# Kernel optimization log

Hardware: AMD Instinct MI355X
Metric: run time of the kernel (lower is better)

Reference implementation:

```python
import jax, jax.numpy as jnp
import numpy as np


def setup_inputs() -> dict:
    key = jax.random.key(0)
    ks = jax.random.split(key, 5)
    B, C, T, Hh, Ww = 4, 64, 8, 32, 32
    HID = 32
    s = 0.05  # weight scale for numerically sane softmax logits
    return {
        "H": jax.random.normal(ks[0], (B, C, T, Hh, Ww), dtype=jnp.float32),
        "h": jax.random.normal(ks[1], (B, C, Hh, Ww), dtype=jnp.float32),
        "w_q": jax.random.normal(ks[2], (HID, C), dtype=jnp.float32) * s,
        "w_kv": jax.random.normal(ks[3], (HID, C), dtype=jnp.float32) * s,
        "w_o": jax.random.normal(ks[4], (C, HID), dtype=jnp.float32) * s,
    }


def reference(H, h, w_q, w_kv, w_o):
    B, C, T, Hh, Ww = H.shape
    N = Hh * Ww
    Hf = H.reshape(B, C, T, N)
    # 1x1 convs are pure channel-mixing matmuls
    H_kv = jnp.einsum('dc,bctn->bdtn', w_kv, Hf)                # [B, hid, T, N]
    h_q = jnp.einsum('dc,bchw->bdhw', w_q, h).reshape(B, -1, N)  # [B, hid, N]
    h_q = h_q.transpose(0, 2, 1)                                 # [B, N, hid]
    # per-timestep scores, vectorized over t: [B, T, N, N]
    a = jnp.einsum('bnd,bdtm->btnm', h_q, H_kv)
    # remove the diagonal of each per-timestep [N, N] block
    diag = jnp.einsum('btnn->btn', a)                            # [B, T, N]
    eye = jnp.eye(N, dtype=a.dtype)
    a = a - diag[..., :, None] * eye
    # concat over t along rows, softmax over the (T*N) row axis
    att = jax.nn.softmax(a.reshape(B, T * N, N), axis=1)         # [B, T*N, N]
    h_v = jnp.einsum('bdk,bkm->bdm', H_kv.reshape(B, -1, T * N), att)  # [B, hid, N]
    h_v = jnp.einsum('cd,bdhw->bchw', w_o, h_v.reshape(B, -1, Hh, Ww))
    return (h + h_v, att)
```

## Files before the change

kernel.cpp:

```cpp
#include <hip/hip_runtime.h>

typedef short bf16x8 __attribute__((ext_vector_type(8)));
typedef float f32x4  __attribute__((ext_vector_type(4)));
typedef unsigned short ushort_t;

#define HID 32
#define CC  64
#define TT  8
#define NN  1024
#define BB  4
#define KTOT 8192
#define NKC_A 16
#define KCHUNK_A (KTOT/NKC_A)
#define NKC_P 32
#define KCHUNK_P (KTOT/NKC_P)

__device__ __forceinline__ ushort_t f2b(float x) {
    unsigned int u = __float_as_uint(x);
    return (ushort_t)((u + 0x7fffu + ((u >> 16) & 1u)) >> 16);
}
__device__ __forceinline__ float b2f(ushort_t u) {
    return __uint_as_float((unsigned int)u << 16);
}

__global__ __launch_bounds__(256) void k_pre(const float* __restrict__ H,
                                             const float* __restrict__ h,
                                             const float* __restrict__ wq,
                                             const float* __restrict__ wkv,
                                             ushort_t* __restrict__ hqHI,
                                             ushort_t* __restrict__ hqLO,
                                             ushort_t* __restrict__ hkTH0,
                                             ushort_t* __restrict__ hkTH1,
                                             ushort_t* __restrict__ hkTL0,
                                             ushort_t* __restrict__ hkTL1,
                                             ushort_t* __restrict__ hkDB) {
    int bx = blockIdx.x;
    if (bx < 256) {
        int gid = bx * 256 + threadIdx.x;
        int dg = gid >> 15;
        int rest = gid & 32767;
        int b = rest >> 13, tn = rest & 8191;
        int d0 = dg << 4;
        float acc[16];
#pragma unroll
        for (int d = 0; d < 16; d++) acc[d] = 0.f;
        const float* Hb = H + (size_t)(b * CC) * KTOT + tn;
        const float* wb = wkv + d0 * CC;
#pragma unroll 16
        for (int c = 0; c < CC; c++) {
            float v = Hb[(size_t)c * KTOT];
#pragma unroll
            for (int d = 0; d < 16; d++) acc[d] += wb[d * CC + c] * v;
        }
        ushort_t thi[16], tlo[16];
#pragma unroll
        for (int d = 0; d < 16; d++) {
            ushort_t hi = f2b(acc[d]);
            thi[d] = hi;
            tlo[d] = f2b(acc[d] - b2f(hi));
        }
        size_t po = ((size_t)b * KTOT + tn) * 16;
        bf16x8* ohi = (bf16x8*)((dg ? hkTH1 : hkTH0) + po);
        bf16x8* olo = (bf16x8*)((dg ? hkTL1 : hkTL0) + po);
#pragma unroll
        for (int v8 = 0; v8 < 2; v8++) {
            bf16x8 a, l;
#pragma unroll
            for (int j = 0; j < 8; j++) { a[j] = (short)thi[v8*8+j]; l[j] = (short)tlo[v8*8+j]; }
            ohi[v8] = a; olo[v8] = l;
        }
#pragma unroll
        for (int d = 0; d < 16; d++)
            hkDB[((size_t)(b * HID) + d0 + d) * KTOT + tn] = thi[d];
    } else {
        int gid = (bx - 256) * 256 + threadIdx.x;
        int b = gid >> 10;
        float acc[HID];
#pragma unroll
        for (int d = 0; d < HID; d++) acc[d] = 0.f;
        const float* hb = h + (size_t)(b * CC) * NN + (gid & 1023);
#pragma unroll 8
        for (int c = 0; c < CC; c++) {
            float v = hb[c * NN];
#pragma unroll
            for (int d = 0; d < HID; d++) acc[d] += wq[d * CC + c] * v;
        }
        bf16x8* ohi = (bf16x8*)(hqHI + (size_t)gid * HID);
        bf16x8* olo = (bf16x8*)(hqLO + (size_t)gid * HID);
#pragma unroll
        for (int v8 = 0; v8 < 4; v8++) {
            bf16x8 thi, tlo;
#pragma unroll
            for (int j = 0; j < 8; j++) {
                float x = acc[v8 * 8 + j];
                ushort_t hi = f2b(x);
                thi[j] = (short)hi;
                tlo[j] = (short)f2b(x - b2f(hi));
            }
            ohi[v8] = thi; olo[v8] = tlo;
        }
    }
}

__global__ __launch_bounds__(256, 8) void k_psum(const ushort_t* __restrict__ hqHI,
                                                 const ushort_t* __restrict__ hqLO,
                                                 const ushort_t* __restrict__ hkTH0,
                                                 const ushort_t* __restrict__ hkTH1,
                                                 const ushort_t* __restrict__ hkTL0,
                                                 const ushort_t* __restrict__ hkTL1,
                                                 float* __restrict__ psum) {
    int bx = blockIdx.x;
    int b = bx >> 9, mt = (bx >> 5) & 15, kc = bx & 31;
    int wave = threadIdx.x >> 6, lane = threadIdx.x & 63;
    int g = lane >> 4, c = lane & 15;
    int m = mt * 64 + wave * 16 + c;
    int t = kc >> 2;
    int nb0 = (kc & 3) << 8;

    size_t bqo = ((size_t)b * KTOT + t * NN + m) * 16 + (g & 1) * 8;
    bf16x8 bqh = *(const bf16x8*)(((g >> 1) ? hkTH1 : hkTH0) + bqo);
    bf16x8 bql = *(const bf16x8*)(((g >> 1) ? hkTL1 : hkTL0) + bqo);

    const ushort_t* qhi = hqHI + ((size_t)(b << 10)) * HID;
    const ushort_t* qlo = hqLO + ((size_t)(b << 10)) * HID;

    float csum0 = 0.f, csum1 = 0.f;
    for (int s16 = 0; s16 < KCHUNK_P / 16; s16 += 2) {
        int nbA = nb0 + s16 * 16;
        int nbB = nbA + 16;
        size_t aoA = (size_t)(nbA + c) * HID + 8 * g;
        size_t aoB = (size_t)(nbB + c) * HID + 8 * g;
        bf16x8 ahA = *(const bf16x8*)(qhi + aoA);
        bf16x8 alA = *(const bf16x8*)(qlo + aoA);
        bf16x8 ahB = *(const bf16x8*)(qhi + aoB);
        bf16x8 alB = *(const bf16x8*)(qlo + aoB);
        f32x4 svA = __builtin_amdgcn_mfma_f32_16x16x32_bf16(ahA, bql, (f32x4){0.f,0.f,0.f,0.f}, 0, 0, 0);
        f32x4 svB = __builtin_amdgcn_mfma_f32_16x16x32_bf16(ahB, bql, (f32x4){0.f,0.f,0.f,0.f}, 0, 0, 0);
        svA = __builtin_amdgcn_mfma_f32_16x16x32_bf16(alA, bqh, svA, 0, 0, 0);
        svB = __builtin_amdgcn_mfma_f32_16x16x32_bf16(alB, bqh, svB, 0, 0, 0);
        svA = __builtin_amdgcn_mfma_f32_16x16x32_bf16(ahA, bqh, svA, 0, 0, 0);
        svB = __builtin_amdgcn_mfma_f32_16x16x32_bf16(ahB, bqh, svB, 0, 0, 0);
        int nrowA = nbA + 4 * g;
        int nrowB = nbB + 4 * g;
#pragma unroll
        for (int r = 0; r < 4; r++) {
            float xA = (nrowA + r == m) ? 0.f : svA[r];
            float xB = (nrowB + r == m) ? 0.f : svB[r];
            csum0 += __expf(xA);
            csum1 += __expf(xB);
        }
    }
    float csum = csum0 + csum1;
    csum += __shfl_xor(csum, 16);
    csum += __shfl_xor(csum, 32);
    if (lane < 16)
        psum[(((size_t)(b * NKC_P + kc)) << 10) + mt * 64 + wave * 16 + lane] = csum;
}

__global__ __launch_bounds__(256, 4) void k_att2(const ushort_t* __restrict__ hqHI,
                                                 const ushort_t* __restrict__ hqLO,
                                                 const ushort_t* __restrict__ hkTH0,
                                                 const ushort_t* __restrict__ hkTH1,
                                                 const ushort_t* __restrict__ hkTL0,
                                                 const ushort_t* __restrict__ hkTL1,
                                                 const ushort_t* __restrict__ hkDB,
                                                 const float* __restrict__ psum,
                                                 float* __restrict__ att,
                                                 float* __restrict__ hvp) {
    int bx = blockIdx.x;
    int b = bx >> 8, mt = (bx >> 4) & 15, kc = bx & 15;
    int wave = threadIdx.x >> 6, lane = threadIdx.x & 63;
    int g = lane >> 4, c = lane & 15;
    int mb = mt * 64 + wave * 16;
    int t = kc >> 1;
    int nb0 = (kc & 1) << 9;

    f32x4 gs = {0.f, 0.f, 0.f, 0.f};
#pragma unroll
    for (int j = 0; j < NKC_P; j++)
        gs += *(const f32x4*)(psum + (((size_t)(b * NKC_P + j)) << 10) + mb + 4 * g);
    f32x4 vinv;
#pragma unroll
    for (int r = 0; r < 4; r++) vinv[r] = 1.0f / gs[r];

    size_t ako = ((size_t)b * KTOT + t * NN + (mb + c)) * 16 + (g & 1) * 8;
    bf16x8 akh = *(const bf16x8*)(((g >> 1) ? hkTH1 : hkTH0) + ako);
    bf16x8 akl = *(const bf16x8*)(((g >> 1) ? hkTL1 : hkTL0) + ako);

    const ushort_t* qhi = hqHI + ((size_t)(b << 10)) * HID;
    const ushort_t* qlo = hqLO + ((size_t)(b << 10)) * HID;
    const ushort_t* vb0 = hkDB + (size_t)(b * HID + c) * KTOT;
    const ushort_t* vb1 = hkDB + (size_t)(b * HID + 16 + c) * KTOT;
    float* attb = att + (size_t)b * KTOT * NN;

    __shared__ __align__(16) ushort_t PT[4][16][40];
    ushort_t (*pt)[40] = PT[wave];

    f32x4 acc0 = {0.f,0.f,0.f,0.f}, acc1 = {0.f,0.f,0.f,0.f};

    for (int ks = 0; ks < KCHUNK_A / 32; ks++) {
        int k0 = kc * KCHUNK_A + ks * 32;
#pragma unroll
        for (int half = 0; half < 2; half++) {
            int nb = nb0 + ks * 32 + half * 16;
            size_t qo = (size_t)(nb + c) * HID + 8 * g;
            bf16x8 qh = *(const bf16x8*)(qhi + qo);
            bf16x8 ql = *(const bf16x8*)(qlo + qo);
            f32x4 sv = __builtin_amdgcn_mfma_f32_16x16x32_bf16(akh, ql, (f32x4){0.f,0.f,0.f,0.f}, 0, 0, 0);
            sv = __builtin_amdgcn_mfma_f32_16x16x32_bf16(akl, qh, sv, 0, 0, 0);
            sv = __builtin_amdgcn_mfma_f32_16x16x32_bf16(akh, qh, sv, 0, 0, 0);
            int n = nb + c;
            float e0, e1, e2, e3;
            {
                float x0 = (n == mb + 4 * g + 0) ? 0.f : sv[0];
                float x1 = (n == mb + 4 * g + 1) ? 0.f : sv[1];
                float x2 = (n == mb + 4 * g + 2) ? 0.f : sv[2];
                float x3 = (n == mb + 4 * g + 3) ? 0.f : sv[3];
                e0 = __expf(x0) * vinv[0];
                e1 = __expf(x1) * vinv[1];
                e2 = __expf(x2) * vinv[2];
                e3 = __expf(x3) * vinv[3];
            }
            f32x4 ev; ev[0] = e0; ev[1] = e1; ev[2] = e2; ev[3] = e3;
            __builtin_nontemporal_store(ev,
                (f32x4*)(attb + (size_t)(t * NN + n) * NN + mb + 4 * g));
            int kl = half * 16 + c;
            pt[4 * g + 0][kl] = f2b(e0);
            pt[4 * g + 1][kl] = f2b(e1);
            pt[4 * g + 2][kl] = f2b(e2);
            pt[4 * g + 3][kl] = f2b(e3);
        }
        bf16x8 pa = *(const bf16x8*)&pt[c][8 * g];
        bf16x8 v0 = *(const bf16x8*)(vb0 + k0 + 8 * g);
        bf16x8 v1 = *(const bf16x8*)(vb1 + k0 + 8 * g);
        acc0 = __builtin_amdgcn_mfma_f32_16x16x32_bf16(pa, v0, acc0, 0, 0, 0);
        acc1 = __builtin_amdgcn_mfma_f32_16x16x32_bf16(pa, v1, acc1, 0, 0, 0);
    }
    float* o = hvp + ((((size_t)(b * NKC_A + kc)) << 10) + mb) * HID;
#pragma unroll
    for (int r = 0; r < 4; r++) {
        o[(size_t)(4 * g + r) * HID + c]      = acc0[r];
        o[(size_t)(4 * g + r) * HID + 16 + c] = acc1[r];
    }
}

__global__ __launch_bounds__(512) void k_out(const float* __restrict__ h,
                                             const float* __restrict__ wo,
                                             const float* __restrict__ hvp,
                                             float* __restrict__ out0) {
    int bx = blockIdx.x;
    int b = bx >> 6, mt = bx & 63;
    int m0 = mt * 16;
    int tid = threadIdx.x;
    __shared__ float hvL[16][33];
    {
        int mm = tid >> 5, d = tid & 31;
        float s = 0.f;
#pragma unroll
        for (int kc = 0; kc < NKC_A; kc++)
            s += hvp[(((size_t)(b * NKC_A + kc)) << 15) + (size_t)(m0 + mm) * HID + d];
        hvL[mm][d] = s;
    }
    __syncthreads();
#pragma unroll
    for (int i0 = 0; i0 < 2; i0++) {
        int i = i0 * 512 + tid;
        int c = i >> 4, mm = i & 15;
        float v = h[(size_t)(b * CC + c) * NN + m0 + mm];
#pragma unroll
        for (int d = 0; d < HID; d++) v += wo[c * HID + d] * hvL[mm][d];
        out0[(size_t)(b * CC + c) * NN + m0 + mm] = v;
    }
}

extern "C" void kernel_launch(void* const* d_in, const int* in_sizes, int n_in,
                              void* d_out, int out_size, void* d_ws, size_t ws_size,
                              hipStream_t stream) {
    const float* H   = (const float*)d_in[0];
    const float* h   = (const float*)d_in[1];
    const float* wq  = (const float*)d_in[2];
    const float* wkv = (const float*)d_in[3];
    const float* wo  = (const float*)d_in[4];

    float* out0 = (float*)d_out;
    float* att  = out0 + (size_t)BB * CC * NN;

    ushort_t* hqHI  = (ushort_t*)d_ws;
    ushort_t* hqLO  = hqHI  + 131072;
    ushort_t* hkTH0 = hqLO  + 131072;
    ushort_t* hkTH1 = hkTH0 + 524288;
    ushort_t* hkTL0 = hkTH1 + 524288;
    ushort_t* hkTL1 = hkTL0 + 524288;
    ushort_t* hkDB  = hkTL1 + 524288;
    float* psum = (float*)(hkDB + 1048576);
    float* hvp  = psum + 131072;

    k_pre <<<272,  256, 0, stream>>>(H, h, wq, wkv, hqHI, hqLO,
                                     hkTH0, hkTH1, hkTL0, hkTL1, hkDB);
    k_psum<<<2048, 256, 0, stream>>>(hqHI, hqLO, hkTH0, hkTH1, hkTL0, hkTL1, psum);
    k_att2<<<1024, 256, 0, stream>>>(hqHI, hqLO, hkTH0, hkTH1, hkTL0, hkTL1, hkDB,
                                     psum, att, hvp);
    k_out <<<256,  512, 0, stream>>>(h, wo, hvp, out0);
}
```

Measured before the change: 102.2 us.

## Fuse column-sum and attention kernels into one block-level kernel with LDS reductions

Merges the softmax partial-sum kernel and the attention/PV kernel into a single 1024-thread kernel. Each block owns 16 query columns and covers all T*N rows across 16 waves. Column sums and hv partials are reduced in shared memory rather than through global scratch buffers. This removes a launch and the psum/hvp round trips, and k_out now reads a single pre-reduced hv. In exchange the grid shrinks to 256 large blocks, which lowers parallelism and occupancy. The k_pre unroll factors are also reduced.

```diff
diff --git a/kernel.cpp b/kernel.cpp
--- a/kernel.cpp
+++ b/kernel.cpp
@@ -10,10 +10,6 @@
 #define NN  1024
 #define BB  4
 #define KTOT 8192
-#define NKC_A 16
-#define KCHUNK_A (KTOT/NKC_A)
-#define NKC_P 32
-#define KCHUNK_P (KTOT/NKC_P)
 
 __device__ __forceinline__ ushort_t f2b(float x) {
     unsigned int u = __float_as_uint(x);
@@ -46,7 +42,7 @@
         for (int d = 0; d < 16; d++) acc[d] = 0.f;
         const float* Hb = H + (size_t)(b * CC) * KTOT + tn;
         const float* wb = wkv + d0 * CC;
-#pragma unroll 16
+#pragma unroll 8
         for (int c = 0; c < CC; c++) {
             float v = Hb[(size_t)c * KTOT];
 #pragma unroll
@@ -79,7 +75,7 @@
 #pragma unroll
         for (int d = 0; d < HID; d++) acc[d] = 0.f;
         const float* hb = h + (size_t)(b * CC) * NN + (gid & 1023);
-#pragma unroll 8
+#pragma unroll 4
         for (int c = 0; c < CC; c++) {
             float v = hb[c * NN];
 #pragma unroll
@@ -102,86 +98,27 @@
     }
 }
 
-__global__ __launch_bounds__(256, 8) void k_psum(const ushort_t* __restrict__ hqHI,
-                                                 const ushort_t* __restrict__ hqLO,
-                                                 const ushort_t* __restrict__ hkTH0,
-                                                 const ushort_t* __restrict__ hkTH1,
-                                                 const ushort_t* __restrict__ hkTL0,
-                                                 const ushort_t* __restrict__ hkTL1,
-                                                 float* __restrict__ psum) {
+__global__ __launch_bounds__(1024) void k_fuse(const ushort_t* __restrict__ hqHI,
+                                               const ushort_t* __restrict__ hqLO,
+                                               const ushort_t* __restrict__ hkTH0,
+                                               const ushort_t* __restrict__ hkTH1,
+                                               const ushort_t* __restrict__ hkTL0,
+                                               const ushort_t* __restrict__ hkTL1,
+                                               const ushort_t* __restrict__ hkDB,
+                                               float* __restrict__ att,
+                                               float* __restrict__ hv2) {
     int bx = blockIdx.x;
-    int b = bx >> 9, mt = (bx >> 5) & 15, kc = bx & 31;
-    int wave = threadIdx.x >> 6, lane = threadIdx.x & 63;
+    int b = bx >> 6, mt = bx & 63;
+    int mb = mt << 4;
+    int tid = threadIdx.x;
+    int wave = tid >> 6, lane = tid & 63;
     int g = lane >> 4, c = lane & 15;
-    int m = mt * 64 + wave * 16 + c;
-    int t = kc >> 2;
-    int nb0 = (kc & 3) << 8;
-
-    size_t bqo = ((size_t)b * KTOT + t * NN + m) * 16 + (g & 1) * 8;
-    bf16x8 bqh = *(const bf16x8*)(((g >> 1) ? hkTH1 : hkTH0) + bqo);
-    bf16x8 bql = *(const bf16x8*)(((g >> 1) ? hkTL1 : hkTL0) + bqo);
-
-    const ushort_t* qhi = hqHI + ((size_t)(b << 10)) * HID;
-    const ushort_t* qlo = hqLO + ((size_t)(b << 10)) * HID;
-
-    float csum0 = 0.f, csum1 = 0.f;
-    for (int s16 = 0; s16 < KCHUNK_P / 16; s16 += 2) {
-        int nbA = nb0 + s16 * 16;
-        int nbB = nbA + 16;
-        size_t aoA = (size_t)(nbA + c) * HID + 8 * g;
-        size_t aoB = (size_t)(nbB + c) * HID + 8 * g;
-        bf16x8 ahA = *(const bf16x8*)(qhi + aoA);
-        bf16x8 alA = *(const bf16x8*)(qlo + aoA);
-        bf16x8 ahB = *(const bf16x8*)(qhi + aoB);
-        bf16x8 alB = *(const bf16x8*)(qlo + aoB);
-        f32x4 svA = __builtin_amdgcn_mfma_f32_16x16x32_bf16(ahA, bql, (f32x4){0.f,0.f,0.f,0.f}, 0, 0, 0);
-        f32x4 svB = __builtin_amdgcn_mfma_f32_16x16x32_bf16(ahB, bql, (f32x4){0.f,0.f,0.f,0.f}, 0, 0, 0);
-        svA = __builtin_amdgcn_mfma_f32_16x16x32_bf16(alA, bqh, svA, 0, 0, 0);
-        svB = __builtin_amdgcn_mfma_f32_16x16x32_bf16(alB, bqh, svB, 0, 0, 0);
-        svA = __builtin_amdgcn_mfma_f32_16x16x32_bf16(ahA, bqh, svA, 0, 0, 0);
-        svB = __builtin_amdgcn_mfma_f32_16x16x32_bf16(ahB, bqh, svB, 0, 0, 0);
-        int nrowA = nbA + 4 * g;
-        int nrowB = nbB + 4 * g;
-#pragma unroll
-        for (int r = 0; r < 4; r++) {
-            float xA = (nrowA + r == m) ? 0.f : svA[r];
-            float xB = (nrowB + r == m) ? 0.f : svB[r];
-            csum0 += __expf(xA);
-            csum1 += __expf(xB);
-        }
-    }
-    float csum = csum0 + csum1;
-    csum += __shfl_xor(csum, 16);
-    csum += __shfl_xor(csum, 32);
-    if (lane < 16)
-        psum[(((size_t)(b * NKC_P + kc)) << 10) + mt * 64 + wave * 16 + lane] = csum;
-}
-
-__global__ __launch_bounds__(256, 4) void k_att2(const ushort_t* __restrict__ hqHI,
-                                                 const ushort_t* __restrict__ hqLO,
-                                                 const ushort_t* __restrict__ hkTH0,
-                                                 const ushort_t* __restrict__ hkTH1,
-                                                 const ushort_t* __restrict__ hkTL0,
-                                                 const ushort_t* __restrict__ hkTL1,
-                                                 const ushort_t* __restrict__ hkDB,
-                                                 const float* __restrict__ psum,
-                                                 float* __restrict__ att,
-                                                 float* __restrict__ hvp) {
-    int bx = blockIdx.x;
-    int b = bx >> 8, mt = (bx >> 4) & 15, kc = bx & 15;
-    int wave = threadIdx.x >> 6, lane = threadIdx.x & 63;
-    int g = lane >> 4, c = lane & 15;
-    int mb = mt * 64 + wave * 16;
-    int t = kc >> 1;
-    int nb0 = (kc & 1) << 9;
-
-    f32x4 gs = {0.f, 0.f, 0.f, 0.f};
-#pragma unroll
-    for (int j = 0; j < NKC_P; j++)
-        gs += *(const f32x4*)(psum + (((size_t)(b * NKC_P + j)) << 10) + mb + 4 * g);
-    f32x4 vinv;
-#pragma unroll
-    for (int r = 0; r < 4; r++) vinv[r] = 1.0f / gs[r];
+    int t = wave >> 1;
+    int nh = (wave & 1) << 9;
+
+    __shared__ float csred[16][16];
+    __shared__ float hvred[16][16][32];
+    __shared__ __align__(16) ushort_t PT[16][16][40];
 
     size_t ako = ((size_t)b * KTOT + t * NN + (mb + c)) * 16 + (g & 1) * 8;
     bf16x8 akh = *(const bf16x8*)(((g >> 1) ? hkTH1 : hkTH0) + ako);
@@ -189,20 +126,57 @@
 
     const ushort_t* qhi = hqHI + ((size_t)(b << 10)) * HID;
     const ushort_t* qlo = hqLO + ((size_t)(b << 10)) * HID;
+
+    f32x4 cs = {0.f, 0.f, 0.f, 0.f};
+    for (int s16 = 0; s16 < 32; s16 += 2) {
+        int nbA = nh + s16 * 16, nbB = nbA + 16;
+        size_t aoA = (size_t)(nbA + c) * HID + 8 * g;
+        size_t aoB = (size_t)(nbB + c) * HID + 8 * g;
+        bf16x8 qhA = *(const bf16x8*)(qhi + aoA);
+        bf16x8 qlA = *(const bf16x8*)(qlo + aoA);
+        bf16x8 qhB = *(const bf16x8*)(qhi + aoB);
+        bf16x8 qlB = *(const bf16x8*)(qlo + aoB);
+        f32x4 svA = __builtin_amdgcn_mfma_f32_16x16x32_bf16(akh, qlA, (f32x4){0.f,0.f,0.f,0.f}, 0, 0, 0);
+        f32x4 svB = __builtin_amdgcn_mfma_f32_16x16x32_bf16(akh, qlB, (f32x4){0.f,0.f,0.f,0.f}, 0, 0, 0);
+        svA = __builtin_amdgcn_mfma_f32_16x16x32_bf16(akl, qhA, svA, 0, 0, 0);
+        svB = __builtin_amdgcn_mfma_f32_16x16x32_bf16(akl, qhB, svB, 0, 0, 0);
+        svA = __builtin_amdgcn_mfma_f32_16x16x32_bf16(akh, qhA, svA, 0, 0, 0);
+        svB = __builtin_amdgcn_mfma_f32_16x16x32_bf16(akh, qhB, svB, 0, 0, 0);
+        int nA = nbA + c, nB = nbB + c;
+#pragma unroll
+        for (int r = 0; r < 4; r++) {
+            float xA = (nA == mb + 4 * g + r) ? 0.f : svA[r];
+            float xB = (nB == mb + 4 * g + r) ? 0.f : svB[r];
+            cs[r] += __expf(xA) + __expf(xB);
+        }
+    }
+#pragma unroll
+    for (int off = 1; off <= 8; off <<= 1) {
+#pragma unroll
+        for (int r = 0; r < 4; r++) cs[r] += __shfl_xor(cs[r], off, 64);
+    }
+    if (c == 0) *(f32x4*)&csred[wave][4 * g] = cs;
+    __syncthreads();
+    f32x4 gs = {0.f, 0.f, 0.f, 0.f};
+#pragma unroll
+    for (int w = 0; w < 16; w++)
+        gs += *(const f32x4*)&csred[w][4 * g];
+    f32x4 vinv;
+#pragma unroll
+    for (int r = 0; r < 4; r++) vinv[r] = 1.0f / gs[r];
+
     const ushort_t* vb0 = hkDB + (size_t)(b * HID + c) * KTOT;
     const ushort_t* vb1 = hkDB + (size_t)(b * HID + 16 + c) * KTOT;
     float* attb = att + (size_t)b * KTOT * NN;
-
-    __shared__ __align__(16) ushort_t PT[4][16][40];
     ushort_t (*pt)[40] = PT[wave];
 
     f32x4 acc0 = {0.f,0.f,0.f,0.f}, acc1 = {0.f,0.f,0.f,0.f};
 
-    for (int ks = 0; ks < KCHUNK_A / 32; ks++) {
-        int k0 = kc * KCHUNK_A + ks * 32;
+    for (int ks = 0; ks < 16; ks++) {
+        int k0 = t * NN + nh + ks * 32;
 #pragma unroll
         for (int half = 0; half < 2; half++) {
-            int nb = nb0 + ks * 32 + half * 16;
+            int nb = nh + ks * 32 + half * 16;
             size_t qo = (size_t)(nb + c) * HID + 8 * g;
             bf16x8 qh = *(const bf16x8*)(qhi + qo);
             bf16x8 ql = *(const bf16x8*)(qlo + qo);
@@ -236,17 +210,25 @@
         acc0 = __builtin_amdgcn_mfma_f32_16x16x32_bf16(pa, v0, acc0, 0, 0, 0);
         acc1 = __builtin_amdgcn_mfma_f32_16x16x32_bf16(pa, v1, acc1, 0, 0, 0);
     }
-    float* o = hvp + ((((size_t)(b * NKC_A + kc)) << 10) + mb) * HID;
+
 #pragma unroll
     for (int r = 0; r < 4; r++) {
-        o[(size_t)(4 * g + r) * HID + c]      = acc0[r];
-        o[(size_t)(4 * g + r) * HID + 16 + c] = acc1[r];
+        hvred[wave][4 * g + r][c]      = acc0[r];
+        hvred[wave][4 * g + r][16 + c] = acc1[r];
+    }
+    __syncthreads();
+    if (tid < 512) {
+        int m = tid >> 5, d = tid & 31;
+        float s = 0.f;
+#pragma unroll
+        for (int w = 0; w < 16; w++) s += hvred[w][m][d];
+        hv2[((size_t)(b << 10) + mb + m) * HID + d] = s;
     }
 }
 
 __global__ __launch_bounds__(512) void k_out(const float* __restrict__ h,
                                              const float* __restrict__ wo,
-                                             const float* __restrict__ hvp,
+                                             const float* __restrict__ hv2,
                                              float* __restrict__ out0) {
     int bx = blockIdx.x;
     int b = bx >> 6, mt = bx & 63;
@@ -255,11 +237,7 @@
     __shared__ float hvL[16][33];
     {
         int mm = tid >> 5, d = tid & 31;
-        float s = 0.f;
-#pragma unroll
-        for (int kc = 0; kc < NKC_A; kc++)
-            s += hvp[(((size_t)(b * NKC_A + kc)) << 15) + (size_t)(m0 + mm) * HID + d];
-        hvL[mm][d] = s;
+        hvL[mm][d] = hv2[((size_t)(b << 10) + m0 + mm) * HID + d];
     }
     __syncthreads();
 #pragma unroll
@@ -292,13 +270,11 @@
     ushort_t* hkTL0 = hkTH1 + 524288;
     ushort_t* hkTL1 = hkTL0 + 524288;
     ushort_t* hkDB  = hkTL1 + 524288;
-    float* psum = (float*)(hkDB + 1048576);
-    float* hvp  = psum + 131072;
-
-    k_pre <<<272,  256, 0, stream>>>(H, h, wq, wkv, hqHI, hqLO,
+    float* hv2  = (float*)(hkDB + 1048576);
+
+    k_pre <<<272, 256,  0, stream>>>(H, h, wq, wkv, hqHI, hqLO,
                                      hkTH0, hkTH1, hkTL0, hkTL1, hkDB);
-    k_psum<<<2048, 256, 0, stream>>>(hqHI, hqLO, hkTH0, hkTH1, hkTL0, hkTL1, psum);
-    k_att2<<<1024, 256, 0, stream>>>(hqHI, hqLO, hkTH0, hkTH1, hkTL0, hkTL1, hkDB,
-                                     psum, att, hvp);
-    k_out <<<256,  512, 0, stream>>>(h, wo, hvp, out0);
-}
+    k_fuse<<<256, 1024, 0, stream>>>(hqHI, hqLO, hkTH0, hkTH1, hkTL0, hkTL1, hkDB,
+                                     att, hv2);
+    k_out <<<256, 512,  0, stream>>>(h, wo, hv2, out0);
+}
```

After: 88.50 us. 13.4% less time.
